# Kernel optimization log

Hardware: AMD Instinct MI355X
Metric: run time of the kernel (lower is better)

## Reference

```python
import jax, jax.numpy as jnp
import numpy as np

N_NODES = 100000
N_EDGES = 1600000
C_IN = 128
C_OUT = 128
BN_EPS = 1e-5


def setup_inputs() -> dict:
    key = jax.random.key(0)
    k = jax.random.split(key, 4)
    x = jax.random.normal(k[0], (N_NODES, C_IN), dtype=jnp.float32)
    edge_index = jax.random.randint(k[1], (2, N_EDGES), 0, N_NODES, dtype=jnp.int32)
    # nn.Linear params (Kaiming-uniform-ish scale)
    lim = 1.0 / np.sqrt(C_IN)
    W = jax.random.uniform(k[2], (C_IN, C_OUT), jnp.float32, -lim, lim)
    b = jnp.zeros((C_OUT,), jnp.float32)
    # BatchNorm (eval mode: running stats)
    gamma = jnp.ones((C_OUT,), jnp.float32)
    beta = jnp.zeros((C_OUT,), jnp.float32)
    running_mean = jnp.zeros((C_OUT,), jnp.float32)
    running_var = jnp.ones((C_OUT,), jnp.float32)
    return {"x": x, "edge_index": edge_index, "W": W, "b": b,
            "gamma": gamma, "beta": beta,
            "running_mean": running_mean, "running_var": running_var}


def reference(x, edge_index, W, b, gamma, beta, running_mean, running_var):
    # Linear projection: [N, C_in] @ [C_in, C_out]
    h = x @ W + b
    in_node, out_node = edge_index[0], edge_index[1]
    # gather edge features then scatter-mean onto destination nodes
    sums = jax.ops.segment_sum(h[in_node], out_node, num_segments=N_NODES)
    cnt = jax.ops.segment_sum(jnp.ones((in_node.shape[0],), h.dtype), out_node,
                              num_segments=N_NODES)
    agg = sums / jnp.maximum(cnt, 1.0)[:, None]  # mean; 0 for isolated nodes
    # BatchNorm1d (eval mode: running stats) + ReLU; dropout is identity in eval
    inv = jax.lax.rsqrt(running_var + BN_EPS)
    out = (agg - running_mean) * (inv * gamma) + beta
    return jax.nn.relu(out)
```

## Files before the change

### kernel.cpp

```cpp
#include <hip/hip_runtime.h>


#define NN 100000
#define NE 1600000
#define CC 128
#define BN_EPS 1e-5f
#define LBLK 1563
#define LSTR 136
#define NBUK 256
#define DPB 391
#define ACH 4096
#define ABLK 391
#define CAP 10240

typedef __attribute__((ext_vector_type(8))) short bf16x8;
typedef __attribute__((ext_vector_type(4))) float f32x4;

static __device__ __forceinline__ short f2bf(float f) {
  union { float f; unsigned u; } v; v.f = f;
  unsigned r = (v.u + 0x7FFF + ((v.u >> 16) & 1)) >> 16;
  return (short)r;
}
static __device__ __forceinline__ float bflo(unsigned p) {
  return __uint_as_float(p << 16);
}
static __device__ __forceinline__ float bfhi(unsigned p) {
  return __uint_as_float(p & 0xffff0000u);
}

static __device__ __forceinline__ int excl_scan256(int* a, int t, int v) {
  a[t] = v;
  __syncthreads();
  for (int d = 1; d < 256; d <<= 1) {
    const int x = (t >= d) ? a[t - d] : 0;
    __syncthreads();
    a[t] += x;
    __syncthreads();
  }
  const int incl = a[t];
  __syncthreads();
  a[t] = incl - v;
  __syncthreads();
  return incl - v;
}

__global__ __launch_bounds__(256) void prep_hist(
    const float* __restrict__ W, const float* __restrict__ bias,
    const float* __restrict__ gamma, const float* __restrict__ beta,
    const float* __restrict__ rmean, const float* __restrict__ rvar,
    const int* __restrict__ ei, short* __restrict__ Wsw,
    float* __restrict__ scsh, int* __restrict__ bhist) {
  __shared__ int lh[NBUK];
  const int t = threadIdx.x;
  const int i = blockIdx.x * 256 + t;
  if (i < CC * CC) {
    const int k = i >> 7, n = i & 127;
    const int nt = n & 7, m = n >> 3;
    const int kb = k >> 5, q = (k >> 3) & 3, j = k & 7;
    Wsw[(size_t)(((nt * 4 + kb) * 64 + (m + 16 * q)) * 8 + j)] = f2bf(W[i]);
  }
  if (i < CC) {
    const float sc = gamma[i] * rsqrtf(rvar[i] + BN_EPS);
    scsh[i] = sc;
    scsh[CC + i] = beta[i] - rmean[i] * sc;
    scsh[2 * CC + i] = bias[i];
  }
  lh[t] = 0;
  __syncthreads();
  const int e0 = blockIdx.x * ACH;
  const int e1 = min(NE, e0 + ACH);
  for (int e = e0 + t; e < e1; e += 256) atomicAdd(&lh[ei[NE + e] / DPB], 1);
  __syncthreads();
  if (lh[t]) atomicAdd(&bhist[t], lh[t]);
}

__global__ __launch_bounds__(256) void scatter_linear(
    const int* __restrict__ ei, const int* __restrict__ bhist,
    int* __restrict__ gcurz, int2* __restrict__ ebuf,
    const float* __restrict__ x, const short* __restrict__ Wsw,
    const float* __restrict__ scsh, short* __restrict__ hout,
    int scat) {
  __shared__ int2 sorted[ACH];
  __shared__ int gsc[NBUK], lh[NBUK], lex[NBUK], rb[NBUK], lc[NBUK];
  const int t = threadIdx.x;

  if (blockIdx.x < scat) {
    const int e0 = blockIdx.x * ACH;
    const int e1 = min(NE, e0 + ACH);
    const int gbase = excl_scan256(gsc, t, bhist[t]);
    lh[t] = 0;
    __syncthreads();
    for (int e = e0 + t; e < e1; e += 256) atomicAdd(&lh[ei[NE + e] / DPB], 1);
    __syncthreads();
    const int vh = lh[t];
    const int lbase = excl_scan256(lex, t, vh);
    lc[t] = lbase;
    if (vh > 0) rb[t] = gbase + atomicAdd(&gcurz[t], vh);
    __syncthreads();
    for (int e = e0 + t; e < e1; e += 256) {
      const int src = ei[e], dst = ei[NE + e];
      const int p = atomicAdd(&lc[dst / DPB], 1);
      sorted[p] = make_int2(src, dst);
    }
    __syncthreads();
    const int n = e1 - e0;
    for (int i = t; i < n; i += 256) {
      const int2 v = sorted[i];
      const int b = v.y / DPB;
      ebuf[rb[b] + (i - lex[b])] = v;
    }
    return;
  }

  short* lsA = (short*)sorted;
  const int n0 = (blockIdx.x - scat) * 64;

#pragma unroll
  for (int j = 0; j < 8; ++j) {
    const int idx = j * 256 + t;
    const int row = idx >> 5, kc4 = idx & 31;
    float4 v = make_float4(0.f, 0.f, 0.f, 0.f);
    if (n0 + row < NN) v = *(const float4*)(x + (size_t)(n0 + row) * CC + kc4 * 4);
    short4 sv;
    sv.x = f2bf(v.x); sv.y = f2bf(v.y); sv.z = f2bf(v.z); sv.w = f2bf(v.w);
    *(short4*)(lsA + row * LSTR + kc4 * 4) = sv;
  }
  __syncthreads();

  const int wave = t >> 6, lane = t & 63;
  const int quad = lane >> 4, m = lane & 15;
  const int rowbase = n0 + wave * 16;

  f32x4 acc[8];
#pragma unroll
  for (int nt = 0; nt < 8; ++nt) acc[nt] = (f32x4){0.f, 0.f, 0.f, 0.f};

#pragma unroll
  for (int kb = 0; kb < 4; ++kb) {
    const bf16x8 a =
        *(const bf16x8*)(lsA + (wave * 16 + m) * LSTR + kb * 32 + quad * 8);
#pragma unroll
    for (int nt = 0; nt < 8; ++nt) {
      bf16x8 bb = *(const bf16x8*)(Wsw + (size_t)(((nt * 4 + kb) * 64 + lane) * 8));
      acc[nt] = __builtin_amdgcn_mfma_f32_16x16x32_bf16(a, bb, acc[nt], 0, 0, 0);
    }
  }

  const float4 b0 = *(const float4*)(scsh + 2 * CC + m * 8);
  const float4 b1 = *(const float4*)(scsh + 2 * CC + m * 8 + 4);
  const float bv[8] = {b0.x, b0.y, b0.z, b0.w, b1.x, b1.y, b1.z, b1.w};

#pragma unroll
  for (int reg = 0; reg < 4; ++reg) {
    const int R = rowbase + quad * 4 + reg;
    if (R >= NN) continue;
    bf16x8 hv;
#pragma unroll
    for (int nt = 0; nt < 8; ++nt) hv[nt] = f2bf(acc[nt][reg] + bv[nt]);
    *(bf16x8*)(hout + (size_t)R * CC + m * 8) = hv;
  }
}

__global__ __launch_bounds__(256) void bucket_to_csr(
    const int2* __restrict__ ebuf, const int* __restrict__ bhist,
    int* __restrict__ off, int* __restrict__ csr) {
  __shared__ int gs[NBUK];
  __shared__ int dh[512];
  __shared__ int s[512];
  __shared__ int lcur[512];
  __shared__ int lcsr[CAP];
  const int b = blockIdx.x, t = threadIdx.x;
  excl_scan256(gs, t, bhist[t]);
  const int segbase = gs[b];
  const int seglen = bhist[b];
  const int lo = b * DPB;
  const int hi = min(NN, lo + DPB);
  const int nd = hi - lo;
  const int2* eb = ebuf + segbase;

  for (int i = t; i < 512; i += 256) dh[i] = 0;
  __syncthreads();
  for (int i = t; i < seglen; i += 256) atomicAdd(&dh[eb[i].y - lo], 1);
  __syncthreads();

  for (int i = t; i < 512; i += 256) s[i] = dh[i];
  __syncthreads();
  for (int d = 1; d < 512; d <<= 1) {
    const int a0 = (t >= d) ? s[t - d] : 0;
    const int a1 = (t + 256 >= d) ? s[t + 256 - d] : 0;
    __syncthreads();
    s[t] += a0;
    s[t + 256] += a1;
    __syncthreads();
  }
  for (int i = t; i < 512; i += 256) lcur[i] = s[i] - dh[i];
  for (int d = t; d < nd; d += 256) off[lo + d] = segbase + (s[d] - dh[d]);
  if (b == NBUK - 1 && t == 0) off[NN] = NE;
  __syncthreads();

  if (seglen <= CAP) {
    for (int i = t; i < seglen; i += 256) {
      const int2 e = eb[i];
      const int p = atomicAdd(&lcur[e.y - lo], 1);
      lcsr[p] = e.x;
    }
    __syncthreads();
    for (int i = t; i < seglen; i += 256) csr[segbase + i] = lcsr[i];
  } else {
    for (int i = t; i < seglen; i += 256) {
      const int2 e = eb[i];
      const int p = atomicAdd(&lcur[e.y - lo], 1);
      csr[segbase + p] = e.x;
    }
  }
}

__global__ __launch_bounds__(256) void gather_bn_relu(
    const short* __restrict__ h, const int* __restrict__ off,
    const int* __restrict__ csr, const float* __restrict__ scsh,
    float* __restrict__ out) {
  const int node = (blockIdx.x * 256 + threadIdx.x) >> 6;
  const int lane = threadIdx.x & 63;
  if (node >= NN) return;
  const int s = off[node], e = off[node + 1];
  const unsigned* hb = (const unsigned*)h;

  float ax = 0.f, ay = 0.f;
  int i = s;
  for (; i + 7 < e; i += 8) {
    const int s0 = csr[i + 0], s1 = csr[i + 1], s2 = csr[i + 2], s3 = csr[i + 3];
    const int s4 = csr[i + 4], s5 = csr[i + 5], s6 = csr[i + 6], s7 = csr[i + 7];
    const unsigned p0 = hb[(size_t)s0 * 64 + lane];
    const unsigned p1 = hb[(size_t)s1 * 64 + lane];
    const unsigned p2 = hb[(size_t)s2 * 64 + lane];
    const unsigned p3 = hb[(size_t)s3 * 64 + lane];
    const unsigned p4 = hb[(size_t)s4 * 64 + lane];
    const unsigned p5 = hb[(size_t)s5 * 64 + lane];
    const unsigned p6 = hb[(size_t)s6 * 64 + lane];
    const unsigned p7 = hb[(size_t)s7 * 64 + lane];
    ax += ((bflo(p0) + bflo(p1)) + (bflo(p2) + bflo(p3))) +
          ((bflo(p4) + bflo(p5)) + (bflo(p6) + bflo(p7)));
    ay += ((bfhi(p0) + bfhi(p1)) + (bfhi(p2) + bfhi(p3))) +
          ((bfhi(p4) + bfhi(p5)) + (bfhi(p6) + bfhi(p7)));
  }
  for (; i + 3 < e; i += 4) {
    const int s0 = csr[i + 0], s1 = csr[i + 1], s2 = csr[i + 2], s3 = csr[i + 3];
    const unsigned p0 = hb[(size_t)s0 * 64 + lane];
    const unsigned p1 = hb[(size_t)s1 * 64 + lane];
    const unsigned p2 = hb[(size_t)s2 * 64 + lane];
    const unsigned p3 = hb[(size_t)s3 * 64 + lane];
    ax += (bflo(p0) + bflo(p1)) + (bflo(p2) + bflo(p3));
    ay += (bfhi(p0) + bfhi(p1)) + (bfhi(p2) + bfhi(p3));
  }
  for (; i < e; ++i) {
    const unsigned p = hb[(size_t)csr[i] * 64 + lane];
    ax += bflo(p);
    ay += bfhi(p);
  }
  const float inv = (e > s) ? 1.0f / (float)(e - s) : 0.0f;
  const float2 sc = *(const float2*)(scsh + 2 * lane);
  const float2 sh = *(const float2*)(scsh + CC + 2 * lane);
  float2 o;
  o.x = fmaxf(0.f, ax * inv * sc.x + sh.x);
  o.y = fmaxf(0.f, ay * inv * sc.y + sh.y);
  *(float2*)(out + (size_t)node * CC + lane * 2) = o;
}

__global__ __launch_bounds__(256) void edge_scatter(
    const float* __restrict__ x, const int* __restrict__ ei,
    float* __restrict__ sums, int* __restrict__ cnt) {
  int gt = blockIdx.x * 256 + threadIdx.x;
  int e = gt >> 5;
  int sub = gt & 31;
  if (e >= NE) return;
  int src = ei[e];
  int dst = ei[NE + e];
  const float4 v = *(const float4*)(x + (size_t)src * CC + sub * 4);
  float* o = sums + (size_t)dst * CC + sub * 4;
  unsafeAtomicAdd(o + 0, v.x);
  unsafeAtomicAdd(o + 1, v.y);
  unsafeAtomicAdd(o + 2, v.z);
  unsafeAtomicAdd(o + 3, v.w);
  if (sub == 0) atomicAdd(cnt + dst, 1);
}

__global__ __launch_bounds__(256) void gemm_bn_relu_fb(
    float* buf, const float* __restrict__ W, const float* __restrict__ bias,
    const float* __restrict__ gamma, const float* __restrict__ beta,
    const float* __restrict__ rmean, const float* __restrict__ rvar,
    const int* __restrict__ cnt) {
  __shared__ float xsT[CC][65];
  const int t = threadIdx.x;
  const int n0 = blockIdx.x * 64;
  for (int j = 0; j < 8; ++j) {
    int i = t + 256 * j;
    int row = i >> 5;
    int ko = (i & 31) * 4;
    float4 v = make_float4(0.f, 0.f, 0.f, 0.f);
    if (n0 + row < NN) v = *(const float4*)(buf + (size_t)(n0 + row) * CC + ko);
    xsT[ko + 0][row] = v.x;
    xsT[ko + 1][row] = v.y;
    xsT[ko + 2][row] = v.z;
    xsT[ko + 3][row] = v.w;
  }
  __syncthreads();
  const int cg = t & 31;
  const int ng8 = (t >> 5) * 8;
  float acc[8][4];
#pragma unroll
  for (int j = 0; j < 8; ++j)
#pragma unroll
    for (int c = 0; c < 4; ++c) acc[j][c] = 0.f;
#pragma unroll 8
  for (int k = 0; k < CC; ++k) {
    const float4 wv = *(const float4*)(W + k * CC + cg * 4);
#pragma unroll
    for (int j = 0; j < 8; ++j) {
      const float xv = xsT[k][ng8 + j];
      acc[j][0] = fmaf(xv, wv.x, acc[j][0]);
      acc[j][1] = fmaf(xv, wv.y, acc[j][1]);
      acc[j][2] = fmaf(xv, wv.z, acc[j][2]);
      acc[j][3] = fmaf(xv, wv.w, acc[j][3]);
    }
  }
  const float4 bb = *(const float4*)(bias + cg * 4);
  const float4 gg = *(const float4*)(gamma + cg * 4);
  const float4 bt = *(const float4*)(beta + cg * 4);
  const float4 mu = *(const float4*)(rmean + cg * 4);
  const float4 vr = *(const float4*)(rvar + cg * 4);
  float sc[4], sh[4];
  sc[0] = gg.x * rsqrtf(vr.x + BN_EPS);
  sc[1] = gg.y * rsqrtf(vr.y + BN_EPS);
  sc[2] = gg.z * rsqrtf(vr.z + BN_EPS);
  sc[3] = gg.w * rsqrtf(vr.w + BN_EPS);
  sh[0] = bt.x - mu.x * sc[0];
  sh[1] = bt.y - mu.y * sc[1];
  sh[2] = bt.z - mu.z * sc[2];
  sh[3] = bt.w - mu.w * sc[3];
#pragma unroll
  for (int j = 0; j < 8; ++j) {
    const int n = n0 + ng8 + j;
    if (n >= NN) continue;
    const int cn = cnt[n];
    const float inv = cn > 0 ? 1.0f / (float)cn : 0.0f;
    const float bsel = cn > 0 ? 1.0f : 0.0f;
    float4 o;
    o.x = fmaxf(0.f, (acc[j][0] * inv + bsel * bb.x) * sc[0] + sh[0]);
    o.y = fmaxf(0.f, (acc[j][1] * inv + bsel * bb.y) * sc[1] + sh[1]);
    o.z = fmaxf(0.f, (acc[j][2] * inv + bsel * bb.z) * sc[2] + sh[2]);
    o.w = fmaxf(0.f, (acc[j][3] * inv + bsel * bb.w) * sc[3] + sh[3]);
    *(float4*)(buf + (size_t)n * CC + cg * 4) = o;
  }
}

extern "C" void kernel_launch(void* const* d_in, const int* in_sizes, int n_in,
                              void* d_out, int out_size, void* d_ws, size_t ws_size,
                              hipStream_t stream) {
  const float* x     = (const float*)d_in[0];
  const int*   ei    = (const int*)d_in[1];
  const float* W     = (const float*)d_in[2];
  const float* bias  = (const float*)d_in[3];
  const float* gamma = (const float*)d_in[4];
  const float* beta  = (const float*)d_in[5];
  const float* rmean = (const float*)d_in[6];
  const float* rvar  = (const float*)d_in[7];
  float* out = (float*)d_out;

  const size_t OFF_B  = 0;
  const size_t BH_B   = 400128;
  const size_t GC_B   = 401152;
  const size_t CSR_B  = 802304;
  const size_t SCSH_B = 7202304;
  const size_t WSW_B  = 7204352;
  const size_t EB_B   = 7237120;
  const size_t H1_B   = 20037120;
  const size_t NEED1  = H1_B + (size_t)NN * CC * 2;
  const size_t NEED2  = EB_B + (size_t)NN * CC * 2;

  if (ws_size >= NEED2) {
    int*   off   = (int*)((char*)d_ws + OFF_B);
    int*   bhist = (int*)((char*)d_ws + BH_B);
    int*   gcurz = (int*)((char*)d_ws + GC_B);
    int*   csr   = (int*)((char*)d_ws + CSR_B);
    float* scsh  = (float*)((char*)d_ws + SCSH_B);
    short* Wsw   = (short*)((char*)d_ws + WSW_B);

    hipMemsetAsync(bhist, 0, 2048, stream);
    prep_hist<<<ABLK, 256, 0, stream>>>(W, bias, gamma, beta, rmean, rvar,
                                        ei, Wsw, scsh, bhist);
    if (ws_size >= NEED1) {
      int2*  ebuf = (int2*)((char*)d_ws + EB_B);
      short* h    = (short*)((char*)d_ws + H1_B);
      scatter_linear<<<ABLK + LBLK, 256, 0, stream>>>(
          ei, bhist, gcurz, ebuf, x, Wsw, scsh, h, ABLK);
      bucket_to_csr<<<NBUK, 256, 0, stream>>>(ebuf, bhist, off, csr);
      gather_bn_relu<<<(NN * 64 + 255) / 256, 256, 0, stream>>>(h, off, csr,
                                                                scsh, out);
    } else {
      int2*  ebuf = (int2*)((char*)d_ws + EB_B);
      short* h    = (short*)((char*)d_ws + EB_B);
      scatter_linear<<<ABLK, 256, 0, stream>>>(
          ei, bhist, gcurz, ebuf, x, Wsw, scsh, h, ABLK);
      bucket_to_csr<<<NBUK, 256, 0, stream>>>(ebuf, bhist, off, csr);
      scatter_linear<<<LBLK, 256, 0, stream>>>(
          ei, bhist, gcurz, ebuf, x, Wsw, scsh, h, 0);
      gather_bn_relu<<<(NN * 64 + 255) / 256, 256, 0, stream>>>(h, off, csr,
                                                                scsh, out);
    }
  } else {
    int* cnt = (int*)d_ws;
    hipMemsetAsync(out, 0, (size_t)NN * CC * sizeof(float), stream);
    hipMemsetAsync(cnt, 0, (size_t)NN * sizeof(int), stream);
    edge_scatter<<<(NE * 32) / 256, 256, 0, stream>>>(x, ei, out, cnt);
    gemm_bn_relu_fb<<<(NN + 63) / 64, 256, 0, stream>>>(
        out, W, bias, gamma, beta, rmean, rvar, cnt);
  }
}
```

Before: 237.4 us.

## Store h in column-group-major layout and split gather across column groups

The linear kernel now writes h as 8 column groups of 16 bf16 values each, where each group is contiguous across all nodes. The gather kernel launches 8 times as many blocks, one per column group. Within a wave, 8 lanes cover the 32-byte slice of a row and 8 edges are processed in parallel, then combined with cross-lane shuffles. The aim is a smaller per-group working set that fits better in cache, plus more edge-level parallelism per node. The cost is that the CSR indices are read eight times and each row access becomes a 32-byte sector gather.

```diff
diff --git a/kernel.cpp b/kernel.cpp
--- a/kernel.cpp
+++ b/kernel.cpp
@@ -150,6 +150,7 @@
   const float4 b1 = *(const float4*)(scsh + 2 * CC + m * 8 + 4);
   const float bv[8] = {b0.x, b0.y, b0.z, b0.w, b1.x, b1.y, b1.z, b1.w};
 
+  short* hg = hout + (size_t)(m >> 1) * (NN * 16) + (m & 1) * 8;
 #pragma unroll
   for (int reg = 0; reg < 4; ++reg) {
     const int R = rowbase + quad * 4 + reg;
@@ -157,7 +158,7 @@
     bf16x8 hv;
 #pragma unroll
     for (int nt = 0; nt < 8; ++nt) hv[nt] = f2bf(acc[nt][reg] + bv[nt]);
-    *(bf16x8*)(hout + (size_t)R * CC + m * 8) = hv;
+    *(bf16x8*)(hg + (size_t)R * 16) = hv;
   }
 }
 
@@ -219,51 +220,43 @@
     const short* __restrict__ h, const int* __restrict__ off,
     const int* __restrict__ csr, const float* __restrict__ scsh,
     float* __restrict__ out) {
-  const int node = (blockIdx.x * 256 + threadIdx.x) >> 6;
+  const int g = blockIdx.x & 7;
+  const int node = (blockIdx.x >> 3) * 4 + (threadIdx.x >> 6);
+  if (node >= NN) return;
   const int lane = threadIdx.x & 63;
-  if (node >= NN) return;
+  const int e8 = lane >> 3, c8 = lane & 7;
   const int s = off[node], e = off[node + 1];
-  const unsigned* hb = (const unsigned*)h;
+  const unsigned* hb = (const unsigned*)h + (size_t)g * (NN * 8) + c8;
 
   float ax = 0.f, ay = 0.f;
-  int i = s;
-  for (; i + 7 < e; i += 8) {
-    const int s0 = csr[i + 0], s1 = csr[i + 1], s2 = csr[i + 2], s3 = csr[i + 3];
-    const int s4 = csr[i + 4], s5 = csr[i + 5], s6 = csr[i + 6], s7 = csr[i + 7];
-    const unsigned p0 = hb[(size_t)s0 * 64 + lane];
-    const unsigned p1 = hb[(size_t)s1 * 64 + lane];
-    const unsigned p2 = hb[(size_t)s2 * 64 + lane];
-    const unsigned p3 = hb[(size_t)s3 * 64 + lane];
-    const unsigned p4 = hb[(size_t)s4 * 64 + lane];
-    const unsigned p5 = hb[(size_t)s5 * 64 + lane];
-    const unsigned p6 = hb[(size_t)s6 * 64 + lane];
-    const unsigned p7 = hb[(size_t)s7 * 64 + lane];
-    ax += ((bflo(p0) + bflo(p1)) + (bflo(p2) + bflo(p3))) +
-          ((bflo(p4) + bflo(p5)) + (bflo(p6) + bflo(p7)));
-    ay += ((bfhi(p0) + bfhi(p1)) + (bfhi(p2) + bfhi(p3))) +
-          ((bfhi(p4) + bfhi(p5)) + (bfhi(p6) + bfhi(p7)));
-  }
-  for (; i + 3 < e; i += 4) {
-    const int s0 = csr[i + 0], s1 = csr[i + 1], s2 = csr[i + 2], s3 = csr[i + 3];
-    const unsigned p0 = hb[(size_t)s0 * 64 + lane];
-    const unsigned p1 = hb[(size_t)s1 * 64 + lane];
-    const unsigned p2 = hb[(size_t)s2 * 64 + lane];
-    const unsigned p3 = hb[(size_t)s3 * 64 + lane];
-    ax += (bflo(p0) + bflo(p1)) + (bflo(p2) + bflo(p3));
-    ay += (bfhi(p0) + bfhi(p1)) + (bfhi(p2) + bfhi(p3));
-  }
-  for (; i < e; ++i) {
-    const unsigned p = hb[(size_t)csr[i] * 64 + lane];
+  int i = s + e8;
+  for (; i + 8 < e; i += 16) {
+    const int s0 = csr[i], s1 = csr[i + 8];
+    const unsigned p0 = hb[(size_t)s0 * 8];
+    const unsigned p1 = hb[(size_t)s1 * 8];
+    ax += bflo(p0) + bflo(p1);
+    ay += bfhi(p0) + bfhi(p1);
+  }
+  if (i < e) {
+    const unsigned p = hb[(size_t)csr[i] * 8];
     ax += bflo(p);
     ay += bfhi(p);
   }
-  const float inv = (e > s) ? 1.0f / (float)(e - s) : 0.0f;
-  const float2 sc = *(const float2*)(scsh + 2 * lane);
-  const float2 sh = *(const float2*)(scsh + CC + 2 * lane);
-  float2 o;
-  o.x = fmaxf(0.f, ax * inv * sc.x + sh.x);
-  o.y = fmaxf(0.f, ay * inv * sc.y + sh.y);
-  *(float2*)(out + (size_t)node * CC + lane * 2) = o;
+#pragma unroll
+  for (int mask = 8; mask <= 32; mask <<= 1) {
+    ax += __shfl_xor(ax, mask);
+    ay += __shfl_xor(ay, mask);
+  }
+  if (e8 == 0) {
+    const float inv = (e > s) ? 1.0f / (float)(e - s) : 0.0f;
+    const int cidx = g * 16 + c8 * 2;
+    const float2 sc = *(const float2*)(scsh + cidx);
+    const float2 sh = *(const float2*)(scsh + CC + cidx);
+    float2 o;
+    o.x = fmaxf(0.f, ax * inv * sc.x + sh.x);
+    o.y = fmaxf(0.f, ay * inv * sc.y + sh.y);
+    *(float2*)(out + (size_t)node * CC + cidx) = o;
+  }
 }
 
 __global__ __launch_bounds__(256) void edge_scatter(
@@ -377,6 +370,8 @@
   const size_t NEED1  = H1_B + (size_t)NN * CC * 2;
   const size_t NEED2  = EB_B + (size_t)NN * CC * 2;
 
+  const int GGRID = ((NN + 3) / 4) * 8;
+
   if (ws_size >= NEED2) {
     int*   off   = (int*)((char*)d_ws + OFF_B);
     int*   bhist = (int*)((char*)d_ws + BH_B);
@@ -394,8 +389,7 @@
       scatter_linear<<<ABLK + LBLK, 256, 0, stream>>>(
           ei, bhist, gcurz, ebuf, x, Wsw, scsh, h, ABLK);
       bucket_to_csr<<<NBUK, 256, 0, stream>>>(ebuf, bhist, off, csr);
-      gather_bn_relu<<<(NN * 64 + 255) / 256, 256, 0, stream>>>(h, off, csr,
-                                                                scsh, out);
+      gather_bn_relu<<<GGRID, 256, 0, stream>>>(h, off, csr, scsh, out);
     } else {
       int2*  ebuf = (int2*)((char*)d_ws + EB_B);
       short* h    = (short*)((char*)d_ws + EB_B);
@@ -404,8 +398,7 @@
       bucket_to_csr<<<NBUK, 256, 0, stream>>>(ebuf, bhist, off, csr);
       scatter_linear<<<LBLK, 256, 0, stream>>>(
           ei, bhist, gcurz, ebuf, x, Wsw, scsh, h, 0);
-      gather_bn_relu<<<(NN * 64 + 255) / 256, 256, 0, stream>>>(h, off, csr,
-                                                                scsh, out);
+      gather_bn_relu<<<GGRID, 256, 0, stream>>>(h, off, csr, scsh, out);
     }
   } else {
     int* cnt = (int*)d_ws;
```

After: 388.8 us. 1.64x slower.
